# Kernel optimization log

Hardware: AMD Instinct MI355X
Metric: run time of the kernel (lower is better)

## Reference

```python
import jax, jax.numpy as jnp
import numpy as np


def setup_inputs() -> dict:
    key = jax.random.key(0)
    k1, k2 = jax.random.split(key)
    y_pred = jax.random.normal(k1, (8192, 2), dtype=jnp.float32)
    y_true = jax.random.normal(k2, (8192, 2), dtype=jnp.float32)
    return {"y_pred": y_pred, "y_true": y_true}


def reference(y_pred, y_true):
    # Flatten to point clouds of 2D points (matches reshape(-1, 2))
    p = y_pred.astype(jnp.float32).reshape(-1, 2)  # [N, 2]
    t = y_true.astype(jnp.float32).reshape(-1, 2)  # [M, 2]
    # Pairwise Euclidean distances via ||p||^2 + ||t||^2 - 2 p.t^T (avoids [N,M,2] diff tensor)
    sq = (
        jnp.sum(p * p, axis=1, keepdims=True)            # [N, 1]
        + jnp.sum(t * t, axis=1)[None, :]                # [1, M]
        - 2.0 * jnp.einsum("nd,md->nm", p, t)          # [N, M]
    )
    d = jnp.sqrt(jnp.maximum(sq, 0.0))  # [N, M]
    min_p2t = jnp.min(d, axis=1)  # [N]
    min_t2p = jnp.min(d, axis=0)  # [M]
    total = jnp.sum(min_p2t) + jnp.sum(min_t2p)
    return total / t.shape[0]
```

## Files before the change

### kernel.cpp

```cpp
#include <hip/hip_runtime.h>
#include <hip/hip_bf16.h>


#define ROWS 8
#define WAVES_PER_BLOCK 4
#define PTS_PER_BLOCK (ROWS * WAVES_PER_BLOCK)
#define MAXB 8192

__global__ __launch_bounds__(256, 2) void chamfer_min_kernel(
    const float2* __restrict__ P, int N,
    const float2* __restrict__ T, int M,
    int blocksP,
    float* __restrict__ block_sums)
{
    __shared__ float2 sB[MAXB];

    const float2* A; const float2* B; int nA, nB; int bid = blockIdx.x;
    if (bid < blocksP) { A = P; nA = N; B = T; nB = M; }
    else               { A = T; nA = M; B = P; nB = N; bid -= blocksP; }

    const int tid  = threadIdx.x;
    const int lane = tid & 63;
    const int wave = tid >> 6;
    const int n0   = (bid * WAVES_PER_BLOCK + wave) * ROWS;

    {
        const float4* B4 = (const float4*)B;
        float4* S4 = (float4*)sB;
        const int nB4 = nB >> 1;
        for (int i = tid; i < nB4; i += 256) S4[i] = B4[i];
        if (nB & 1) { if (tid == 0) sB[nB - 1] = B[nB - 1]; }
    }

    float m2px[ROWS], m2py[ROWS], pp[ROWS];
    #pragma unroll
    for (int r = 0; r < ROWS; ++r) {
        float2 p;
        if (n0 + r < nA) p = A[n0 + r];
        else             p = make_float2(0.0f, 0.0f);
        m2px[r] = -2.0f * p.x;
        m2py[r] = -2.0f * p.y;
        pp[r]   = fmaf(p.x, p.x, p.y * p.y);
    }

    float g[ROWS];
    #pragma unroll
    for (int r = 0; r < ROWS; ++r) g[r] = 3.402823466e+38f;

    __syncthreads();

    #pragma unroll 4
    for (int m = lane; m < nB; m += 64) {
        float2 t = sB[m];
        float tt = fmaf(t.x, t.x, t.y * t.y);
        #pragma unroll
        for (int r = 0; r < ROWS; ++r) {
            float h = fmaf(m2px[r], t.x, fmaf(m2py[r], t.y, tt));
            g[r] = fminf(g[r], h);
        }
    }

    #pragma unroll
    for (int r = 0; r < ROWS; ++r) {
        float v = g[r];
        #pragma unroll
        for (int off = 32; off >= 1; off >>= 1)
            v = fminf(v, __shfl_xor(v, off, 64));
        g[r] = v;
    }

    __shared__ float wsum[WAVES_PER_BLOCK];
    if (lane == 0) {
        float s = 0.0f;
        #pragma unroll
        for (int r = 0; r < ROWS; ++r)
            if (n0 + r < nA) s += sqrtf(fmaxf(pp[r] + g[r], 0.0f));
        wsum[wave] = s;
    }
    __syncthreads();
    if (tid == 0) {
        float s = 0.0f;
        #pragma unroll
        for (int w = 0; w < WAVES_PER_BLOCK; ++w) s += wsum[w];
        block_sums[blockIdx.x] = s;
    }
}

__global__ __launch_bounds__(256) void final_reduce_kernel(
    const float* __restrict__ sums, int n, float inv_M, float* __restrict__ out)
{
    const int tid = threadIdx.x;
    float s = 0.0f;
    for (int i = tid; i < n; i += 256) s += sums[i];
    #pragma unroll
    for (int off = 32; off >= 1; off >>= 1) s += __shfl_xor(s, off, 64);
    __shared__ float wsum[4];
    if ((tid & 63) == 0) wsum[tid >> 6] = s;
    __syncthreads();
    if (tid == 0) out[0] = (wsum[0] + wsum[1] + wsum[2] + wsum[3]) * inv_M;
}

extern "C" void kernel_launch(void* const* d_in, const int* in_sizes, int n_in,
                              void* d_out, int out_size, void* d_ws, size_t ws_size,
                              hipStream_t stream) {
    const float2* P = (const float2*)d_in[0];
    const float2* T = (const float2*)d_in[1];
    const int N = in_sizes[0] / 2;
    const int M = in_sizes[1] / 2;

    float* out = (float*)d_out;
    float* block_sums = (float*)d_ws;

    const int blocksP = (N + PTS_PER_BLOCK - 1) / PTS_PER_BLOCK;
    const int blocksT = (M + PTS_PER_BLOCK - 1) / PTS_PER_BLOCK;
    const int total_blocks = blocksP + blocksT;

    chamfer_min_kernel<<<total_blocks, 256, 0, stream>>>(P, N, T, M, blocksP, block_sums);
    final_reduce_kernel<<<1, 256, 0, stream>>>(block_sums, total_blocks, 1.0f / (float)M, out);
}
```

Baseline: 20.78 us.

## Fuse final reduction via last-block atomic counter, double waves, vectorize LDS reads

Moves the final sum into the main kernel: each block increments a global atomic counter and the last block to finish reduces all block sums, so the separate reduce launch is gone. It also doubles waves per block to 8, which halves the grid and the redundant shared-memory loads of the other cloud. The inner loop now reads two target points per float4 LDS load. The cost is a memset launch for the counter, threadfence/atomic ordering, and possibly lower occupancy because the launch-bounds minimum is dropped and blocks are larger.

```diff
diff --git a/kernel.cpp b/kernel.cpp
--- a/kernel.cpp
+++ b/kernel.cpp
@@ -3,17 +3,23 @@
 
 
 #define ROWS 8
-#define WAVES_PER_BLOCK 4
+#define WAVES_PER_BLOCK 8
+#define THREADS (WAVES_PER_BLOCK * 64)
 #define PTS_PER_BLOCK (ROWS * WAVES_PER_BLOCK)
 #define MAXB 8192
 
-__global__ __launch_bounds__(256, 2) void chamfer_min_kernel(
+__global__ __launch_bounds__(THREADS) void chamfer_fused_kernel(
     const float2* __restrict__ P, int N,
     const float2* __restrict__ T, int M,
     int blocksP,
-    float* __restrict__ block_sums)
+    float* __restrict__ block_sums,
+    unsigned int* __restrict__ counter,
+    float inv_M,
+    float* __restrict__ out)
 {
     __shared__ float2 sB[MAXB];
+    __shared__ float wsum[WAVES_PER_BLOCK];
+    __shared__ bool isLast;
 
     const float2* A; const float2* B; int nA, nB; int bid = blockIdx.x;
     if (bid < blocksP) { A = P; nA = N; B = T; nB = M; }
@@ -28,8 +34,8 @@
         const float4* B4 = (const float4*)B;
         float4* S4 = (float4*)sB;
         const int nB4 = nB >> 1;
-        for (int i = tid; i < nB4; i += 256) S4[i] = B4[i];
-        if (nB & 1) { if (tid == 0) sB[nB - 1] = B[nB - 1]; }
+        for (int i = tid; i < nB4; i += THREADS) S4[i] = B4[i];
+        if ((nB & 1) && tid == 0) sB[nB - 1] = B[nB - 1];
     }
 
     float m2px[ROWS], m2py[ROWS], pp[ROWS];
@@ -49,14 +55,27 @@
 
     __syncthreads();
 
-    #pragma unroll 4
-    for (int m = lane; m < nB; m += 64) {
-        float2 t = sB[m];
-        float tt = fmaf(t.x, t.x, t.y * t.y);
-        #pragma unroll
-        for (int r = 0; r < ROWS; ++r) {
-            float h = fmaf(m2px[r], t.x, fmaf(m2py[r], t.y, tt));
-            g[r] = fminf(g[r], h);
+    {
+        const float4* S4 = (const float4*)sB;
+        const int nB4 = nB >> 1;
+        #pragma unroll 2
+        for (int m = lane; m < nB4; m += 64) {
+            float4 tc = S4[m];
+            float tt0 = fmaf(tc.x, tc.x, tc.y * tc.y);
+            float tt1 = fmaf(tc.z, tc.z, tc.w * tc.w);
+            #pragma unroll
+            for (int r = 0; r < ROWS; ++r) {
+                float h0 = fmaf(m2px[r], tc.x, fmaf(m2py[r], tc.y, tt0));
+                float h1 = fmaf(m2px[r], tc.z, fmaf(m2py[r], tc.w, tt1));
+                g[r] = fminf(g[r], fminf(h0, h1));
+            }
+        }
+        if (nB & 1) {
+            float2 t = sB[nB - 1];
+            float tt = fmaf(t.x, t.x, t.y * t.y);
+            #pragma unroll
+            for (int r = 0; r < ROWS; ++r)
+                g[r] = fminf(g[r], fmaf(m2px[r], t.x, fmaf(m2py[r], t.y, tt)));
         }
     }
 
@@ -69,7 +88,6 @@
         g[r] = v;
     }
 
-    __shared__ float wsum[WAVES_PER_BLOCK];
     if (lane == 0) {
         float s = 0.0f;
         #pragma unroll
@@ -83,21 +101,28 @@
         #pragma unroll
         for (int w = 0; w < WAVES_PER_BLOCK; ++w) s += wsum[w];
         block_sums[blockIdx.x] = s;
+        __threadfence();
+        unsigned int old = atomicAdd(counter, 1u);
+        isLast = (old == gridDim.x - 1);
     }
-}
+    __syncthreads();
 
-__global__ __launch_bounds__(256) void final_reduce_kernel(
-    const float* __restrict__ sums, int n, float inv_M, float* __restrict__ out)
-{
-    const int tid = threadIdx.x;
-    float s = 0.0f;
-    for (int i = tid; i < n; i += 256) s += sums[i];
-    #pragma unroll
-    for (int off = 32; off >= 1; off >>= 1) s += __shfl_xor(s, off, 64);
-    __shared__ float wsum[4];
-    if ((tid & 63) == 0) wsum[tid >> 6] = s;
-    __syncthreads();
-    if (tid == 0) out[0] = (wsum[0] + wsum[1] + wsum[2] + wsum[3]) * inv_M;
+    if (isLast) {
+        __threadfence();
+        float s = 0.0f;
+        for (int i = tid; i < (int)gridDim.x; i += THREADS) s += block_sums[i];
+        #pragma unroll
+        for (int off = 32; off >= 1; off >>= 1) s += __shfl_xor(s, off, 64);
+        __shared__ float fsum[WAVES_PER_BLOCK];
+        if (lane == 0) fsum[wave] = s;
+        __syncthreads();
+        if (tid == 0) {
+            float tot = 0.0f;
+            #pragma unroll
+            for (int w = 0; w < WAVES_PER_BLOCK; ++w) tot += fsum[w];
+            out[0] = tot * inv_M;
+        }
+    }
 }
 
 extern "C" void kernel_launch(void* const* d_in, const int* in_sizes, int n_in,
@@ -110,11 +135,14 @@
 
     float* out = (float*)d_out;
     float* block_sums = (float*)d_ws;
+    unsigned int* counter = (unsigned int*)((char*)d_ws + 4096);
 
     const int blocksP = (N + PTS_PER_BLOCK - 1) / PTS_PER_BLOCK;
     const int blocksT = (M + PTS_PER_BLOCK - 1) / PTS_PER_BLOCK;
     const int total_blocks = blocksP + blocksT;
 
-    chamfer_min_kernel<<<total_blocks, 256, 0, stream>>>(P, N, T, M, blocksP, block_sums);
-    final_reduce_kernel<<<1, 256, 0, stream>>>(block_sums, total_blocks, 1.0f / (float)M, out);
+    hipMemsetAsync(counter, 0, sizeof(unsigned int), stream);
+
+    chamfer_fused_kernel<<<total_blocks, THREADS, 0, stream>>>(
+        P, N, T, M, blocksP, block_sums, counter, 1.0f / (float)M, out);
 }
```

Measured after the change: 29.03 us. +39.7%, slower.

## Use 1024-thread blocks with fewer rows per wave and float4 LDS reads

Applied to the files above, without the earlier changes.

Each block now has 16 waves of 4 rows instead of 4 waves of 8 rows. That halves the block count, so the full 64KB target cloud is staged into LDS half as often, and each CU holds more resident waves. The inner loop reads two points per float4 LDS load and folds both candidates into the running min with a nested fminf, which may compile to min3. The trade-off is fewer rows reusing each LDS value, so each wave issues more LDS reads, and only one block fits per CU.

```diff
diff --git a/kernel.cpp b/kernel.cpp
--- a/kernel.cpp
+++ b/kernel.cpp
@@ -2,18 +2,20 @@
 #include <hip/hip_bf16.h>
 
 
-#define ROWS 8
-#define WAVES_PER_BLOCK 4
+#define ROWS 4
+#define WAVES_PER_BLOCK 16
+#define THREADS (WAVES_PER_BLOCK * 64)
 #define PTS_PER_BLOCK (ROWS * WAVES_PER_BLOCK)
 #define MAXB 8192
 
-__global__ __launch_bounds__(256, 2) void chamfer_min_kernel(
+__global__ __launch_bounds__(THREADS) void chamfer_min_kernel(
     const float2* __restrict__ P, int N,
     const float2* __restrict__ T, int M,
     int blocksP,
     float* __restrict__ block_sums)
 {
     __shared__ float2 sB[MAXB];
+    __shared__ float wsum[WAVES_PER_BLOCK];
 
     const float2* A; const float2* B; int nA, nB; int bid = blockIdx.x;
     if (bid < blocksP) { A = P; nA = N; B = T; nB = M; }
@@ -28,8 +30,8 @@
         const float4* B4 = (const float4*)B;
         float4* S4 = (float4*)sB;
         const int nB4 = nB >> 1;
-        for (int i = tid; i < nB4; i += 256) S4[i] = B4[i];
-        if (nB & 1) { if (tid == 0) sB[nB - 1] = B[nB - 1]; }
+        for (int i = tid; i < nB4; i += THREADS) S4[i] = B4[i];
+        if ((nB & 1) && tid == 0) sB[nB - 1] = B[nB - 1];
     }
 
     float m2px[ROWS], m2py[ROWS], pp[ROWS];
@@ -49,14 +51,27 @@
 
     __syncthreads();
 
-    #pragma unroll 4
-    for (int m = lane; m < nB; m += 64) {
-        float2 t = sB[m];
-        float tt = fmaf(t.x, t.x, t.y * t.y);
-        #pragma unroll
-        for (int r = 0; r < ROWS; ++r) {
-            float h = fmaf(m2px[r], t.x, fmaf(m2py[r], t.y, tt));
-            g[r] = fminf(g[r], h);
+    {
+        const float4* S4 = (const float4*)sB;
+        const int nB4 = nB >> 1;
+        #pragma unroll 4
+        for (int m = lane; m < nB4; m += 64) {
+            float4 tc = S4[m];
+            float tt0 = fmaf(tc.x, tc.x, tc.y * tc.y);
+            float tt1 = fmaf(tc.z, tc.z, tc.w * tc.w);
+            #pragma unroll
+            for (int r = 0; r < ROWS; ++r) {
+                float h0 = fmaf(m2px[r], tc.x, fmaf(m2py[r], tc.y, tt0));
+                float h1 = fmaf(m2px[r], tc.z, fmaf(m2py[r], tc.w, tt1));
+                g[r] = fminf(fminf(g[r], h0), h1);
+            }
+        }
+        if (nB & 1) {
+            float2 t = sB[nB - 1];
+            float tt = fmaf(t.x, t.x, t.y * t.y);
+            #pragma unroll
+            for (int r = 0; r < ROWS; ++r)
+                g[r] = fminf(g[r], fmaf(m2px[r], t.x, fmaf(m2py[r], t.y, tt)));
         }
     }
 
@@ -69,7 +84,6 @@
         g[r] = v;
     }
 
-    __shared__ float wsum[WAVES_PER_BLOCK];
     if (lane == 0) {
         float s = 0.0f;
         #pragma unroll
@@ -115,6 +129,6 @@
     const int blocksT = (M + PTS_PER_BLOCK - 1) / PTS_PER_BLOCK;
     const int total_blocks = blocksP + blocksT;
 
-    chamfer_min_kernel<<<total_blocks, 256, 0, stream>>>(P, N, T, M, blocksP, block_sums);
+    chamfer_min_kernel<<<total_blocks, THREADS, 0, stream>>>(P, N, T, M, blocksP, block_sums);
     final_reduce_kernel<<<1, 256, 0, stream>>>(block_sums, total_blocks, 1.0f / (float)M, out);
 }
```

Result: faster. 18.30 us (-11.9%).
